# Kernel tuning notes

Hardware: AMD Instinct MI355X
Metric: run time of the kernel (lower is better)

Reference implementation:

```python
import jax, jax.numpy as jnp
import numpy as np

N9, N10, F = 6000, 9000, 128
ALPHA = 0.2  # LeakyReLU negative slope
NEG_INF = -9e15


def setup_inputs() -> dict:
    key = jax.random.key(0)
    k1, k2, k3, k4, k5 = jax.random.split(key, 5)
    U_9 = jax.random.normal(k1, (N9, F), dtype=jnp.float32) * 0.03
    U_10 = jax.random.normal(k2, (N10, F), dtype=jnp.float32) * 0.03
    # xavier_uniform with gain=1.414 for a: limit = gain*sqrt(6/(fan_in+fan_out))
    lim = 1.414 * np.sqrt(6.0 / (2 * F + 1))
    a = jax.random.uniform(k3, (2 * F, 1), dtype=jnp.float32, minval=-lim, maxval=lim)
    # sparse 0/1 code-mapping adjacencies, avg degree ~4
    adj_9to10 = (jax.random.uniform(k4, (N9, N10)) < 4.0 / N10).astype(jnp.float32)
    adj_10to9 = (jax.random.uniform(k5, (N10, N9)) < 4.0 / N9).astype(jnp.float32)
    return {"version": 0, "U_9": U_9, "U_10": U_10, "a": a,
            "adj_9to10": adj_9to10, "adj_10to9": adj_10to9}


def _gat(query, key_feat, adj, a):
    # a splits into the query-half and key-half of the attention vector
    Fd = query.shape[1]
    a1 = a[:Fd, 0]   # [F]
    a2 = a[Fd:, 0]   # [F]
    qa1 = query @ a1        # [Nq]
    qa2 = query @ a2        # [Nq]
    ka2 = key_feat @ a2     # [Nk]
    # self column: leakyrelu([q, q] @ a)
    self_e = jax.nn.leaky_relu(qa1 + qa2, ALPHA)                 # [Nq]
    # cross scores at edge positions: leakyrelu(q_i.a1 + k_j.a2);
    # non-edge entries differ from the torch sparse->dense zeros but are
    # masked to -9e15 below, so the output math is identical.
    e_cross = jax.nn.leaky_relu(qa1[:, None] + ka2[None, :], ALPHA)  # [Nq, Nk]
    ones_col = jnp.ones((query.shape[0], 1), dtype=adj.dtype)
    adj_full = jnp.concatenate([ones_col, adj], axis=1)          # [Nq, Nk+1]
    scores = jnp.concatenate([self_e[:, None], e_cross], axis=1)  # [Nq, Nk+1]
    scores = jnp.where(adj_full > 0, scores, NEG_INF)
    attn = jax.nn.softmax(scores, axis=-1) * adj_full
    attn = jnp.where(jnp.isnan(attn), 0.0, attn)
    h_prime = attn[:, :1] * query + attn[:, 1:] @ key_feat       # [Nq, F]
    return jax.nn.elu(h_prime)


def reference(version, U_9, U_10, a, adj_9to10, adj_10to9):
    if version == 0:  # 'mimiciv_icd9'
        return _gat(U_9, U_10, adj_9to10, a)
    else:
        return _gat(U_10, U_9, adj_10to9, a)
```

## Files before the change

### kernel.cpp

```cpp
#include <hip/hip_runtime.h>
#include <math.h>

#define N9   6000
#define N10  9000
#define FDIM 128
#define ALPHA 0.2f
#define MAXNBR 1024

__global__ __launch_bounds__(64)
void gat_dots_kernel(const int* __restrict__ version,
                     const float* __restrict__ U9,
                     const float* __restrict__ U10,
                     const float* __restrict__ a,
                     float* __restrict__ qa1,
                     float* __restrict__ qa2,
                     float* __restrict__ ka2) {
    const int v  = version[0];
    const int nq = v ? N10 : N9;
    const int nk = v ? N9  : N10;
    const float* __restrict__ Q = v ? U10 : U9;
    const float* __restrict__ K = v ? U9  : U10;
    const float* __restrict__ a1 = a;
    const float* __restrict__ a2 = a + FDIM;

    const int row  = blockIdx.x;
    const int lane = threadIdx.x;

    if (row < nq) {
        const float* x = Q + (size_t)row * FDIM;
        float x0 = x[lane], x1 = x[lane + 64];
        float s1 = x0 * a1[lane] + x1 * a1[lane + 64];
        float s2 = x0 * a2[lane] + x1 * a2[lane + 64];
        #pragma unroll
        for (int o = 32; o > 0; o >>= 1) {
            s1 += __shfl_down(s1, o);
            s2 += __shfl_down(s2, o);
        }
        if (lane == 0) { qa1[row] = s1; qa2[row] = s2; }
    } else {
        const int r = row - nq;
        if (r < nk) {
            const float* x = K + (size_t)r * FDIM;
            float s2 = x[lane] * a2[lane] + x[lane + 64] * a2[lane + 64];
            #pragma unroll
            for (int o = 32; o > 0; o >>= 1) s2 += __shfl_down(s2, o);
            if (lane == 0) ka2[r] = s2;
        }
    }
}

__global__ __launch_bounds__(256)
void gat_row_kernel(const int* __restrict__ version,
                    const float* __restrict__ U9,
                    const float* __restrict__ U10,
                    const float* __restrict__ adj9to10,
                    const float* __restrict__ adj10to9,
                    const float* __restrict__ qa1,
                    const float* __restrict__ qa2,
                    const float* __restrict__ ka2,
                    float* __restrict__ out) {
    const int v  = version[0];
    const int nq = v ? N10 : N9;
    const int nk = v ? N9  : N10;
    const int i  = blockIdx.x;
    if (i >= nq) return;

    const float* __restrict__ Q   = v ? U10 : U9;
    const float* __restrict__ K   = v ? U9  : U10;
    const float* __restrict__ adj = (v ? adj10to9 : adj9to10) + (size_t)i * nk;

    __shared__ int   s_cnt;
    __shared__ float s_wself;
    __shared__ int   s_j[MAXNBR];
    __shared__ float s_e[MAXNBR];
    __shared__ float s_w[MAXNBR];

    const int t = threadIdx.x;
    if (t == 0) s_cnt = 0;
    __syncthreads();

    const float qa1i = qa1[i];

    const float4* __restrict__ adj4 = (const float4*)adj;
    const int n4 = nk >> 2;
    for (int p = t; p < n4; p += 256) {
        float4 vv = adj4[p];
        if (vv.x > 0.f || vv.y > 0.f || vv.z > 0.f || vv.w > 0.f) {
            float va[4] = {vv.x, vv.y, vv.z, vv.w};
            #pragma unroll
            for (int c = 0; c < 4; ++c) {
                if (va[c] > 0.f) {
                    int idx = atomicAdd(&s_cnt, 1);
                    if (idx < MAXNBR) {
                        int j = p * 4 + c;
                        float e = qa1i + ka2[j];
                        e = (e >= 0.f) ? e : ALPHA * e;
                        s_j[idx] = j;
                        s_e[idx] = e;
                    }
                }
            }
        }
    }
    __syncthreads();

    const int cnt = (s_cnt < MAXNBR) ? s_cnt : MAXNBR;

    if (t == 0) {
        float se = qa1i + qa2[i];
        se = (se >= 0.f) ? se : ALPHA * se;
        float m = se;
        for (int c = 0; c < cnt; ++c) m = fmaxf(m, s_e[c]);
        float wself = expf(se - m);
        float wsum  = wself;
        for (int c = 0; c < cnt; ++c) {
            float w = expf(s_e[c] - m);
            s_w[c] = w;
            wsum += w;
        }
        float inv = 1.f / wsum;
        s_wself = wself * inv;
        for (int c = 0; c < cnt; ++c) s_w[c] *= inv;
    }
    __syncthreads();

    if (t < FDIM) {
        float h = s_wself * Q[(size_t)i * FDIM + t];
        for (int c = 0; c < cnt; ++c) {
            h += s_w[c] * K[(size_t)s_j[c] * FDIM + t];
        }
        h = (h > 0.f) ? h : expm1f(h);
        out[(size_t)i * FDIM + t] = h;
    }
}

extern "C" void kernel_launch(void* const* d_in, const int* in_sizes, int n_in,
                              void* d_out, int out_size, void* d_ws, size_t ws_size,
                              hipStream_t stream) {
    const int*   d_version = (const int*)d_in[0];
    const float* d_U9      = (const float*)d_in[1];
    const float* d_U10     = (const float*)d_in[2];
    const float* d_a       = (const float*)d_in[3];
    const float* d_adj9    = (const float*)d_in[4];
    const float* d_adj10   = (const float*)d_in[5];
    float*       d_o       = (float*)d_out;

    float* w_qa1 = (float*)d_ws;
    float* w_qa2 = w_qa1 + N10;
    float* w_ka2 = w_qa2 + N10;

    gat_dots_kernel<<<N9 + N10, 64, 0, stream>>>(
        d_version, d_U9, d_U10, d_a, w_qa1, w_qa2, w_ka2);

    gat_row_kernel<<<N10, 256, 0, stream>>>(
        d_version, d_U9, d_U10, d_adj9, d_adj10,
        w_qa1, w_qa2, w_ka2, d_o);
}
```

Before: 48.49 us.

## Use persistent grid-stride row blocks with unrolled adjacency loads

```diff
diff --git a/kernel.cpp b/kernel.cpp
--- a/kernel.cpp
+++ b/kernel.cpp
@@ -5,7 +5,8 @@
 #define N10  9000
 #define FDIM 128
 #define ALPHA 0.2f
-#define MAXNBR 1024
+#define MAXNBR 128
+#define ROWBLOCKS 2048
 
 __global__ __launch_bounds__(64)
 void gat_dots_kernel(const int* __restrict__ version,
@@ -62,12 +63,10 @@
     const int v  = version[0];
     const int nq = v ? N10 : N9;
     const int nk = v ? N9  : N10;
-    const int i  = blockIdx.x;
-    if (i >= nq) return;
 
-    const float* __restrict__ Q   = v ? U10 : U9;
-    const float* __restrict__ K   = v ? U9  : U10;
-    const float* __restrict__ adj = (v ? adj10to9 : adj9to10) + (size_t)i * nk;
+    const float* __restrict__ Q      = v ? U10 : U9;
+    const float* __restrict__ K      = v ? U9  : U10;
+    const float* __restrict__ adjmat = v ? adj10to9 : adj9to10;
 
     __shared__ int   s_cnt;
     __shared__ float s_wself;
@@ -75,62 +74,79 @@
     __shared__ float s_e[MAXNBR];
     __shared__ float s_w[MAXNBR];
 
-    const int t = threadIdx.x;
-    if (t == 0) s_cnt = 0;
-    __syncthreads();
+    const int t  = threadIdx.x;
+    const int n4 = nk >> 2;
 
-    const float qa1i = qa1[i];
+    for (int i = blockIdx.x; i < nq; i += gridDim.x) {
+        if (t == 0) s_cnt = 0;
+        __syncthreads();
 
-    const float4* __restrict__ adj4 = (const float4*)adj;
-    const int n4 = nk >> 2;
-    for (int p = t; p < n4; p += 256) {
-        float4 vv = adj4[p];
-        if (vv.x > 0.f || vv.y > 0.f || vv.z > 0.f || vv.w > 0.f) {
-            float va[4] = {vv.x, vv.y, vv.z, vv.w};
+        const float qa1i = qa1[i];
+        const float4* __restrict__ adj4 = (const float4*)(adjmat + (size_t)i * nk);
+
+        for (int p0 = t; p0 < n4; p0 += 256 * 4) {
+            const int p1 = p0 + 256, p2 = p0 + 512, p3 = p0 + 768;
+            float4 r0 = adj4[p0];
+            float4 r1 = make_float4(0.f, 0.f, 0.f, 0.f);
+            float4 r2 = r1, r3 = r1;
+            if (p1 < n4) r1 = adj4[p1];
+            if (p2 < n4) r2 = adj4[p2];
+            if (p3 < n4) r3 = adj4[p3];
+
+            float4 rr[4] = {r0, r1, r2, r3};
+            int    pp[4] = {p0, p1, p2, p3};
             #pragma unroll
-            for (int c = 0; c < 4; ++c) {
-                if (va[c] > 0.f) {
-                    int idx = atomicAdd(&s_cnt, 1);
-                    if (idx < MAXNBR) {
-                        int j = p * 4 + c;
-                        float e = qa1i + ka2[j];
-                        e = (e >= 0.f) ? e : ALPHA * e;
-                        s_j[idx] = j;
-                        s_e[idx] = e;
+            for (int u = 0; u < 4; ++u) {
+                float4 vv = rr[u];
+                if (vv.x > 0.f || vv.y > 0.f || vv.z > 0.f || vv.w > 0.f) {
+                    float va[4] = {vv.x, vv.y, vv.z, vv.w};
+                    #pragma unroll
+                    for (int c = 0; c < 4; ++c) {
+                        if (va[c] > 0.f) {
+                            int idx = atomicAdd(&s_cnt, 1);
+                            if (idx < MAXNBR) {
+                                int j = pp[u] * 4 + c;
+                                float e = qa1i + ka2[j];
+                                e = (e >= 0.f) ? e : ALPHA * e;
+                                s_j[idx] = j;
+                                s_e[idx] = e;
+                            }
+                        }
                     }
                 }
             }
         }
-    }
-    __syncthreads();
+        __syncthreads();
 
-    const int cnt = (s_cnt < MAXNBR) ? s_cnt : MAXNBR;
+        const int cnt = (s_cnt < MAXNBR) ? s_cnt : MAXNBR;
 
-    if (t == 0) {
-        float se = qa1i + qa2[i];
-        se = (se >= 0.f) ? se : ALPHA * se;
-        float m = se;
-        for (int c = 0; c < cnt; ++c) m = fmaxf(m, s_e[c]);
-        float wself = expf(se - m);
-        float wsum  = wself;
-        for (int c = 0; c < cnt; ++c) {
-            float w = expf(s_e[c] - m);
-            s_w[c] = w;
-            wsum += w;
+        if (t == 0) {
+            float se = qa1i + qa2[i];
+            se = (se >= 0.f) ? se : ALPHA * se;
+            float m = se;
+            for (int c = 0; c < cnt; ++c) m = fmaxf(m, s_e[c]);
+            float wself = expf(se - m);
+            float wsum  = wself;
+            for (int c = 0; c < cnt; ++c) {
+                float w = expf(s_e[c] - m);
+                s_w[c] = w;
+                wsum += w;
+            }
+            float inv = 1.f / wsum;
+            s_wself = wself * inv;
+            for (int c = 0; c < cnt; ++c) s_w[c] *= inv;
         }
-        float inv = 1.f / wsum;
-        s_wself = wself * inv;
-        for (int c = 0; c < cnt; ++c) s_w[c] *= inv;
-    }
-    __syncthreads();
+        __syncthreads();
 
-    if (t < FDIM) {
-        float h = s_wself * Q[(size_t)i * FDIM + t];
-        for (int c = 0; c < cnt; ++c) {
-            h += s_w[c] * K[(size_t)s_j[c] * FDIM + t];
+        if (t < FDIM) {
+            float h = s_wself * Q[(size_t)i * FDIM + t];
+            for (int c = 0; c < cnt; ++c) {
+                h += s_w[c] * K[(size_t)s_j[c] * FDIM + t];
+            }
+            h = (h > 0.f) ? h : expm1f(h);
+            out[(size_t)i * FDIM + t] = h;
         }
-        h = (h > 0.f) ? h : expm1f(h);
-        out[(size_t)i * FDIM + t] = h;
+        __syncthreads();
     }
 }
 
@@ -152,7 +168,7 @@
     gat_dots_kernel<<<N9 + N10, 64, 0, stream>>>(
         d_version, d_U9, d_U10, d_a, w_qa1, w_qa2, w_ka2);
 
-    gat_row_kernel<<<N10, 256, 0, stream>>>(
+    gat_row_kernel<<<ROWBLOCKS, 256, 0, stream>>>(
         d_version, d_U9, d_U10, d_adj9, d_adj10,
         w_qa1, w_qa2, w_ka2, d_o);
 }
```

After: 48.38 us. About the same (-0.2%).
